# Kernel tuning notes

Hardware: AMD Instinct MI355X
Metric: run time of the kernel (lower is better)

Reference implementation:

```python
import jax, jax.numpy as jnp
import numpy as np


def _lstm_cell(x, h, c, Wih, Whh, b):
    # torch LSTM gate order: i, f, g, o
    g = x @ Wih.T + h @ Whh.T + b
    i, f, gg, o = jnp.split(g, 4, axis=-1)
    c = jax.nn.sigmoid(f) * c + jax.nn.sigmoid(i) * jnp.tanh(gg)
    h = jax.nn.sigmoid(o) * jnp.tanh(c)
    return h, c


def _run_lstm(emb, mask, Wih, Whh, b, reverse):
    # mask-gated scan emulates pack_padded_sequence: state frozen on pad steps,
    # final (h, c) equals state at last valid token of each sequence.
    B = emb.shape[0]
    H = Whh.shape[1]
    def step(carry, inp):
        h, c = carry
        x, m = inp  # x: (B, E), m: (B, 1)
        hn, cn = _lstm_cell(x, h, c, Wih, Whh, b)
        h = m * hn + (1.0 - m) * h
        c = m * cn + (1.0 - m) * c
        return (h, c), h
    xs = (jnp.swapaxes(emb, 0, 1), jnp.swapaxes(mask, 0, 1)[..., None])
    z = jnp.zeros((B, H), emb.dtype)
    (h, c), outs = jax.lax.scan(step, (z, z), xs, reverse=reverse)
    return jnp.swapaxes(outs, 0, 1), h, c  # (B, T, H), (B, H), (B, H)


def setup_inputs() -> dict:
    key = jax.random.key(0)
    ks = iter(jax.random.split(key, 40))
    B, Te, Td, E, H, Ve, Vd = 32, 64, 32, 256, 512, 32000, 32000
    s = 0.05
    def rn(shape):
        return jax.random.normal(next(ks), shape, jnp.float32) * s
    def zz(n):
        return jnp.zeros((n,), jnp.float32)
    return {
        "enc_texts": jax.random.randint(next(ks), (B, Te), 0, Ve),
        "enc_mask": jnp.ones((B, Te), jnp.float32),
        "dec_texts": jax.random.randint(next(ks), (B, Td), 0, Vd),
        "enc_emb": rn((Ve, E)),
        "dec_emb": rn((Vd, E)),
        "Wih_f": rn((4 * H, E)), "Whh_f": rn((4 * H, H)), "b_f": zz(4 * H),
        "Wih_b": rn((4 * H, E)), "Whh_b": rn((4 * H, H)), "b_b": zz(4 * H),
        "Wih_d": rn((4 * H, E + 2 * H)), "Whh_d": rn((4 * H, H)), "b_d": zz(4 * H),
        "W_h": rn((H, 2 * H)), "b_h": zz(H),
        "W_c": rn((H, 2 * H)), "b_c": zz(H),
        "W_df": rn((2 * H, 2 * H)), "b_df": zz(2 * H),
        "W_ef": rn((2 * H, 2 * H)), "b_ef": zz(2 * H),
        "W_out": rn((Vd, 3 * H)), "b_out": zz(Vd),
    }


def reference(enc_texts, enc_mask, dec_texts, enc_emb, dec_emb,
              Wih_f, Whh_f, b_f, Wih_b, Whh_b, b_b,
              Wih_d, Whh_d, b_d, W_h, b_h, W_c, b_c,
              W_df, b_df, W_ef, b_ef, W_out, b_out):
    B = enc_texts.shape[0]
    H = Whh_d.shape[1]
    # ---- encode: bidirectional LSTM over embedded source ----
    emb = enc_emb[enc_texts]  # (B, Te, E)
    out_f, hf, cf = _run_lstm(emb, enc_mask, Wih_f, Whh_f, b_f, reverse=False)
    out_b, hb, cb = _run_lstm(emb, enc_mask, Wih_b, Whh_b, b_b, reverse=True)
    enc_output = jnp.concatenate([out_f, out_b], -1) * enc_mask[..., None]  # (B, Te, 2H)
    # ---- decode_init: project concat of directional final states ----
    dec_h = jax.nn.relu(jnp.concatenate([hf, hb], -1) @ W_h.T + b_h)  # (B, H)
    dec_c = jax.nn.relu(jnp.concatenate([cf, cb], -1) @ W_c.T + b_c)  # (B, H)
    # precompute attention keys once (enc_output_fc)
    enc_feat = enc_output @ W_ef.T + b_ef  # (B, Te, 2H)
    # teacher-forcing inputs: tokens 0..Td-2
    dec_in = dec_emb[dec_texts[:, :-1]]  # (B, Td-1, E)
    ctx0 = jnp.zeros((B, 2 * H), enc_output.dtype)

    def step(carry, x):
        h, c, ctx = carry
        xin = jnp.concatenate([x, ctx], -1)  # (B, E + 2H)
        h, c = _lstm_cell(xin, h, c, Wih_d, Whh_d, b_d)
        # dot attention: query from projected (h, c)
        df = jnp.concatenate([h, c], -1) @ W_df.T + b_df  # (B, 2H)
        scores = jnp.einsum('bd,btd->bt', df, enc_feat)
        a = jax.nn.softmax(scores, axis=-1) * enc_mask
        a = a / jnp.sum(a, axis=-1, keepdims=True)
        ctx = jnp.einsum('bt,btd->bd', a, enc_output)  # (B, 2H)
        logits = jnp.concatenate([h, ctx], -1) @ W_out.T + b_out  # (B, Vd)
        return (h, c, ctx), logits

    _, logits = jax.lax.scan(step, (dec_h, dec_c, ctx0), jnp.swapaxes(dec_in, 0, 1))
    return jnp.swapaxes(logits, 0, 1)  # (B, Td-1, Vd)
```

## Files before the change

### kernel.cpp

```cpp
#include <hip/hip_runtime.h>
#include <hip/hip_bf16.h>


typedef __attribute__((ext_vector_type(8))) short bfrag_t;
typedef __attribute__((ext_vector_type(4))) float f4_t;

static __device__ __forceinline__ float bf2f(unsigned short u) {
  union { float f; unsigned int i; } v; v.i = ((unsigned int)u) << 16; return v.f;
}
static __device__ __forceinline__ unsigned short f2bf(float f) {
  union { float f; unsigned int i; } v; v.f = f;
  unsigned int r = v.i + 0x7FFFu + ((v.i >> 16) & 1u);
  return (unsigned short)(r >> 16);
}
static __device__ __forceinline__ unsigned int pack_bf2(float lo, float hi) {
  __hip_bfloat162 h2 = __float22bfloat162_rn(make_float2(lo, hi));
  union { __hip_bfloat162 h; unsigned int u; } cv; cv.h = h2;
  return cv.u;
}
static __device__ __forceinline__ float sigm(float x) {
  return __builtin_amdgcn_rcpf(1.f + __expf(-x));
}
static __device__ __forceinline__ float ftanh(float x) {
  float e = __expf(2.f * x);
  return 1.f - 2.f * __builtin_amdgcn_rcpf(e + 1.f);
}

#define GLDS16(g, l)                                                        \
  __builtin_amdgcn_global_load_lds(                                         \
      (const __attribute__((address_space(1))) void*)(g),                   \
      (__attribute__((address_space(3))) void*)(l), 16, 0, 0)

static __device__ __forceinline__ void st_f32_coh(float* p, float v) {
  asm volatile("global_store_dword %0, %1, off sc0 sc1" :: "v"(p), "v"(v) : "memory");
}
static __device__ __forceinline__ void st_u16_coh(unsigned short* p, unsigned short x) {
  asm volatile("global_store_short %0, %1, off sc0 sc1" :: "v"(p), "v"((unsigned)x) : "memory");
}
static __device__ __forceinline__ float ld_f32_coh(const float* p) {
  float v;
  asm volatile("global_load_dword %0, %1, off sc0 sc1\n\ts_waitcnt vmcnt(0)"
               : "=v"(v) : "v"(p) : "memory");
  return v;
}

static __device__ __forceinline__ void arrive8(unsigned* base) {
  __syncthreads();
  if (threadIdx.x == 0)
    __hip_atomic_fetch_add(base + (blockIdx.x & 7) * 32, 1u,
                           __ATOMIC_RELAXED, __HIP_MEMORY_SCOPE_AGENT);
}
static __device__ __forceinline__ void wait8(unsigned* base, unsigned target) {
  if (threadIdx.x < 64) {
    unsigned sum;
    do {
      unsigned v = 0;
      if (threadIdx.x < 8)
        v = __hip_atomic_load(base + threadIdx.x * 32,
                              __ATOMIC_RELAXED, __HIP_MEMORY_SCOPE_AGENT);
      v += __shfl_xor(v, 1);
      v += __shfl_xor(v, 2);
      v += __shfl_xor(v, 4);
      sum = __shfl(v, 0);
      if (sum < target) __builtin_amdgcn_s_sleep(2);
    } while (sum < target);
  }
  __syncthreads();
}
static __device__ __forceinline__ void gbar8(unsigned* base, unsigned target) {
  arrive8(base);
  wait8(base, target);
}

__global__ __launch_bounds__(256) void gemm_bt_kernel(
    const unsigned short* __restrict__ A, int lda,
    const float* __restrict__ B, int ldb, int bcol0,
    const float* __restrict__ bias, void* __restrict__ Cv, int ldc,
    int Mvalid, int K, int Mt, int swz, int obf) {
  __shared__ unsigned short As[128 * 32];
  __shared__ unsigned short Bs[128 * 32];
  int id = blockIdx.x;
  if (swz) { int x = id & 7; id = x * ((int)gridDim.x >> 3) + (id >> 3); }
  const int mb = id % Mt, nb = id / Mt;
  const int m0 = mb * 128, n0 = nb * 128;
  const int tid = threadIdx.x;
  const int w = tid >> 6, lane = tid & 63;
  const int wr = (w >> 1) * 64, wc = (w & 1) * 64;
  const int l15 = lane & 15, l4 = lane >> 4;

  const int arow = w * 16 + (lane >> 2);
  const int acol = (lane & 3) * 8;
  const unsigned short* Ag = A + (size_t)(m0 + arow) * lda + acol;

  const int brow = tid >> 1;
  const int bcol = (tid & 1) * 16;
  const float* Bg = B + (size_t)(n0 + brow) * ldb + bcol0 + bcol;
  unsigned short* Bsw = Bs + brow * 32 + bcol;

  f4_t acc[4][4];
#pragma unroll
  for (int i = 0; i < 4; ++i)
#pragma unroll
    for (int j = 0; j < 4; ++j) {
      acc[i][j].x = 0.f; acc[i][j].y = 0.f; acc[i][j].z = 0.f; acc[i][j].w = 0.f;
    }

  for (int kt = 0; kt < K; kt += 32) {
    GLDS16(Ag + kt, As + w * 512);
    GLDS16(Ag + (size_t)64 * lda + kt, As + (4 + w) * 512);
    float4 q0 = *(const float4*)(Bg + kt);
    float4 q1 = *(const float4*)(Bg + kt + 4);
    float4 q2 = *(const float4*)(Bg + kt + 8);
    float4 q3 = *(const float4*)(Bg + kt + 12);
    union { unsigned int u[8]; uint4 q[2]; } pk;
    pk.u[0] = pack_bf2(q0.x, q0.y); pk.u[1] = pack_bf2(q0.z, q0.w);
    pk.u[2] = pack_bf2(q1.x, q1.y); pk.u[3] = pack_bf2(q1.z, q1.w);
    pk.u[4] = pack_bf2(q2.x, q2.y); pk.u[5] = pack_bf2(q2.z, q2.w);
    pk.u[6] = pack_bf2(q3.x, q3.y); pk.u[7] = pack_bf2(q3.z, q3.w);
    *(uint4*)(Bsw) = pk.q[0];
    *(uint4*)(Bsw + 8) = pk.q[1];
    __syncthreads();
    bfrag_t af[4], bfv[4];
#pragma unroll
    for (int m = 0; m < 4; ++m)
      af[m] = *(const bfrag_t*)(As + (wr + m * 16 + l15) * 32 + l4 * 8);
#pragma unroll
    for (int n = 0; n < 4; ++n)
      bfv[n] = *(const bfrag_t*)(Bs + (wc + n * 16 + l15) * 32 + l4 * 8);
#pragma unroll
    for (int m = 0; m < 4; ++m)
#pragma unroll
      for (int n = 0; n < 4; ++n)
        acc[m][n] = __builtin_amdgcn_mfma_f32_16x16x32_bf16(af[m], bfv[n], acc[m][n], 0, 0, 0);
    __syncthreads();
  }

  const int crb = l4 * 4;
  float* Cf = (float*)Cv;
  unsigned short* Ch = (unsigned short*)Cv;
#pragma unroll
  for (int m = 0; m < 4; ++m)
#pragma unroll
    for (int n = 0; n < 4; ++n)
#pragma unroll
      for (int r = 0; r < 4; ++r) {
        int gr = m0 + wr + m * 16 + crb + r;
        if (gr < Mvalid) {
          int gc = n0 + wc + n * 16 + l15;
          float v = acc[m][n][r] + (bias ? bias[gc] : 0.f);
          if (obf) Ch[(size_t)gr * ldc + gc] = f2bf(v);
          else     Cf[(size_t)gr * ldc + gc] = v;
        }
      }
}

__global__ void gather_enc_kernel(const int* __restrict__ texts,
                                  const float* __restrict__ table,
                                  unsigned short* __restrict__ out) {
  const int row = blockIdx.x;
  const int tok = texts[row];
  const float4 v = *(const float4*)(table + (size_t)tok * 256 + threadIdx.x * 4);
  unsigned short* o = out + (size_t)row * 256 + threadIdx.x * 4;
  o[0] = f2bf(v.x); o[1] = f2bf(v.y); o[2] = f2bf(v.z); o[3] = f2bf(v.w);
}

__global__ void gather_dec_kernel(const int* __restrict__ texts,
                                  const float* __restrict__ table,
                                  unsigned short* __restrict__ out) {
  const int row = blockIdx.x;
  unsigned short* o = out + (size_t)row * 256 + threadIdx.x * 4;
  if (row >= 992) { o[0] = 0; o[1] = 0; o[2] = 0; o[3] = 0; return; }
  const int b = row / 31, t2 = row - b * 31;
  const int tok = texts[b * 32 + t2];
  const float4 v = *(const float4*)(table + (size_t)tok * 256 + threadIdx.x * 4);
  o[0] = f2bf(v.x); o[1] = f2bf(v.y); o[2] = f2bf(v.z); o[3] = f2bf(v.w);
}

__global__ __launch_bounds__(256) void wdf_t_kernel(
    const float* __restrict__ W_df, const float* __restrict__ b_df,
    float* __restrict__ WT) {
  const int bid = blockIdx.x;
  if (bid < 1024) {
    __shared__ float tl[32][33];
    const int tx = (bid & 31) * 32, ty = (bid >> 5) * 32;
    const int r = threadIdx.x >> 5, c = threadIdx.x & 31;
#pragma unroll
    for (int i = 0; i < 4; ++i)
      tl[r + i * 8][c] = W_df[(size_t)(ty + r + i * 8) * 1024 + tx + c];
    __syncthreads();
#pragma unroll
    for (int i = 0; i < 4; ++i)
      WT[(size_t)(tx + r + i * 8) * 1024 + ty + c] = tl[c][r + i * 8];
  } else {
    for (int i = threadIdx.x; i < 1024; i += 256)
      WT[(size_t)1024 * 1024 + i] = b_df[i];
  }
}

__global__ __launch_bounds__(256) void mega_enc_kernel(
    const float* __restrict__ XF, const float* __restrict__ XB,
    const float* __restrict__ Whh_f, const float* __restrict__ Whh_b,
    const float* __restrict__ mask,
    unsigned short* __restrict__ HBF,
    unsigned short* __restrict__ ENCO, float* __restrict__ HFIN,
    unsigned* bar) {
  const int bi = blockIdx.x;
  const int dir = bi >> 6;
  const int u0 = (bi & 63) * 8;
  const int tid = threadIdx.x;
  const float* X = dir ? XB : XF;
  const float* W = dir ? Whh_b : Whh_f;
  unsigned short* Hbf = HBF + dir * 32768;
  unsigned* cnt = bar + dir * 256;

  __shared__ unsigned short WA[32 * 520];
  __shared__ unsigned short HB[32 * 520];
  __shared__ float Gl[32][33];

#pragma unroll
  for (int i = 0; i < 16; ++i) {
    int idx = tid + i * 256;
    int r = idx >> 7, c4 = idx & 127;
    const float4 v = *(const float4*)(W + (size_t)((r >> 3) * 512 + u0 + (r & 7)) * 512 + c4 * 4);
    *(uint2*)(WA + r * 520 + c4 * 4) = make_uint2(pack_bf2(v.x, v.y), pack_bf2(v.z, v.w));
  }
  __syncthreads();

  const int w = tid >> 6, lane = tid & 63;
  const int l15 = lane & 15, l4 = lane >> 4;
  const int wrow = (w >> 1) * 16, wcol = (w & 1) * 16;

  bfrag_t afr[16];
#pragma unroll
  for (int kk = 0; kk < 16; ++kk)
    afr[kk] = *(const bfrag_t*)(WA + (wrow + l15) * 520 + kk * 32 + l4 * 8);

  const int ob = tid & 31, ouo = tid >> 5;
  const int ou = u0 + ouo;
  float h_reg = 0.f, c_reg = 0.f;

  unsigned tgt = 0;
  for (int s = 0; s < 64; ++s) {
    const int t = dir ? (63 - s) : s;
    const int pp = s & 1;
    const float* xp = X + ((size_t)ob * 64 + t) * 2048 + ou;
    float xg0 = xp[0], xg1 = xp[512], xg2 = xp[1024], xg3 = xp[1536];
    float mval = mask[ob * 64 + t];
    const unsigned short* hsrc = Hbf + pp * 16384;
    uint4 tmp[8];
#pragma unroll
    for (int i = 0; i < 8; ++i) {
      int idx = tid + i * 256;
      int r = idx >> 6, c = idx & 63;
      asm volatile("global_load_dwordx4 %0, %1, off sc0 sc1"
                   : "=v"(tmp[i]) : "v"(hsrc + r * 512 + c * 8));
    }
    asm volatile("s_waitcnt vmcnt(0)" ::: "memory");
#pragma unroll
    for (int i = 0; i < 8; ++i) {
      int idx = tid + i * 256;
      int r = idx >> 6, c = idx & 63;
      *(uint4*)(HB + r * 520 + c * 8) = tmp[i];
    }
    __syncthreads();
    {
      f4_t ae = {0.f, 0.f, 0.f, 0.f}, ao = {0.f, 0.f, 0.f, 0.f};
#pragma unroll
      for (int kk = 0; kk < 16; kk += 2) {
        bfrag_t b0 = *(const bfrag_t*)(HB + (wcol + l15) * 520 + kk * 32 + l4 * 8);
        bfrag_t b1 = *(const bfrag_t*)(HB + (wcol + l15) * 520 + (kk + 1) * 32 + l4 * 8);
        ae = __builtin_amdgcn_mfma_f32_16x16x32_bf16(afr[kk], b0, ae, 0, 0, 0);
        ao = __builtin_amdgcn_mfma_f32_16x16x32_bf16(afr[kk + 1], b1, ao, 0, 0, 0);
      }
#pragma unroll
      for (int r = 0; r < 4; ++r)
        Gl[wrow + l4 * 4 + r][wcol + l15] = ae[r] + ao[r];
    }
    __syncthreads();
    {
      float gi = Gl[ouo][ob] + xg0;
      float gf = Gl[8 + ouo][ob] + xg1;
      float gg = Gl[16 + ouo][ob] + xg2;
      float go = Gl[24 + ouo][ob] + xg3;
      float cn = sigm(gf) * c_reg + sigm(gi) * ftanh(gg);
      float hn = sigm(go) * ftanh(cn);
      float hmix = mval * hn + (1.f - mval) * h_reg;
      float cmix = mval * cn + (1.f - mval) * c_reg;
      h_reg = hmix; c_reg = cmix;
      ENCO[((size_t)ob * 64 + t) * 1024 + dir * 512 + ou] = f2bf(hmix * mval);
      st_u16_coh(Hbf + (pp ^ 1) * 16384 + ob * 512 + ou, f2bf(hmix));
      if (s == 63) {
        HFIN[dir * 16384 + ob * 512 + ou] = hmix;
        HFIN[(2 + dir) * 16384 + ob * 512 + ou] = cmix;
      }
    }
    if (s < 63) { tgt += 64; gbar8(cnt, tgt); }
  }
}

__global__ __launch_bounds__(256) void mega_dec_kernel(
    const float* __restrict__ HFIN, const float* __restrict__ W_h,
    const float* __restrict__ b_h, const float* __restrict__ W_c,
    const float* __restrict__ b_c, const float* __restrict__ XD,
    const float* __restrict__ Wih_d, const float* __restrict__ Whh_d,
    const unsigned short* __restrict__ EFG, const unsigned short* __restrict__ ENCO,
    const float* __restrict__ mask, float* __restrict__ DECH,
    float* __restrict__ DECC, unsigned short* __restrict__ PRE0,
    unsigned short* __restrict__ ACAT, unsigned* bar) {
  const int bi = blockIdx.x;
  const int tid = threadIdx.x;
  const bool is_attn = (bi >= 128);
  const int u0 = bi * 4;
  unsigned* barB1 = bar;
  unsigned* barB2 = bar + 256;

  __shared__ union {
    struct {
      unsigned short wga[16 * 1544];
      unsigned short xb[32 * 1544];
      float gl[16][33];
    } s;
    struct {
      unsigned short efg[64 * 1160];
      float hcl[1024];
      float scl[64];
      float al[64];
    } a;
    struct { float xl[32][132]; float wi[8][132]; } ini;
  } U;

  const int ob = tid & 31, ouo = (tid >> 5) & 3, ou = u0 + ouo;
  const int w = tid >> 6, lane = tid & 63;
  const int l15 = lane & 15, l4 = lane >> 4;

  if (!is_attn) {
    {
      const int mat = bi >> 6, j0i = (bi & 63) * 8;
      const int jj = tid >> 5, b = tid & 31;
      const int sr = tid >> 5, sc = (tid & 31) * 4;
      const float* Wm = mat ? W_c : W_h;
      const float* bias = mat ? b_c : b_h;
      const float* x0 = HFIN + (size_t)(mat ? 2 : 0) * 16384;
      const float* x1 = HFIN + (size_t)(mat ? 3 : 1) * 16384;
      float acc = 0.f;
      for (int kc = 0; kc < 1024; kc += 128) {
#pragma unroll
        for (int i = 0; i < 4; ++i) {
          int r = sr + i * 8;
          const float* src = (kc < 512) ? (x0 + r * 512 + kc + sc)
                                        : (x1 + r * 512 + (kc - 512) + sc);
          *(float4*)&U.ini.xl[r][sc] = *(const float4*)src;
        }
        *(float4*)&U.ini.wi[sr][sc] = *(const float4*)(Wm + (size_t)(j0i + sr) * 1024 + kc + sc);
        __syncthreads();
#pragma unroll
        for (int k = 0; k < 128; k += 4) {
          float4 wv = *(const float4*)&U.ini.wi[jj][k];
          float4 xv = *(const float4*)&U.ini.xl[b][k];
          acc += wv.x * xv.x + wv.y * xv.y + wv.z * xv.z + wv.w * xv.w;
        }
        __syncthreads();
      }
      float v = fmaxf(acc + bias[j0i + jj], 0.f);
      if (mat == 0) {
        st_f32_coh(DECH + b * 512 + j0i + jj, v);
        st_u16_coh(PRE0 + (size_t)b * 1536 + j0i + jj, f2bf(v));
      } else {
        st_f32_coh(DECC + b * 512 + j0i + jj, v);
      }
    }
    arrive8(barB1);
    wait8(barB1, 128);

#pragma unroll
    for (int i = 0; i < 24; ++i) {
      int idx = tid + i * 256;
      int r = idx / 384, c4 = idx - (idx / 384) * 384;
      int wrow = (r >> 2) * 512 + u0 + (r & 3);
      int c = c4 * 4;
      float4 v;
      if (c < 512) v = *(const float4*)(Whh_d + (size_t)wrow * 512 + c);
      else         v = *(const float4*)(Wih_d + (size_t)wrow * 1280 + 256 + (c - 512));
      *(uint2*)(U.s.wga + r * 1544 + c) = make_uint2(pack_bf2(v.x, v.y), pack_bf2(v.z, v.w));
    }
    float h_reg = 0.f, c_reg = 0.f;
    if (tid < 128) {
      h_reg = ld_f32_coh(DECH + ob * 512 + ou);
      c_reg = ld_f32_coh(DECC + ob * 512 + ou);
    }

    f4_t cae = {0.f, 0.f, 0.f, 0.f}, cao = {0.f, 0.f, 0.f, 0.f};

    for (int t = 0; t < 31; ++t) {
      float xg0 = 0, xg1 = 0, xg2 = 0, xg3 = 0;
      if (tid < 128) {
        const float* xp = XD + ((size_t)ob * 31 + t) * 2048 + ou;
        xg0 = xp[0]; xg1 = xp[512]; xg2 = xp[1024]; xg3 = xp[1536];
      }
      if (t == 0) {
        uint4 tmp[24];
#pragma unroll
        for (int i = 0; i < 24; ++i) {
          int idx = tid + i * 256;
          int r = idx / 192, c16 = idx - (idx / 192) * 192;
          asm volatile("global_load_dwordx4 %0, %1, off sc0 sc1"
                       : "=v"(tmp[i]) : "v"(PRE0 + (size_t)r * 1536 + c16 * 8));
        }
        asm volatile("s_waitcnt vmcnt(0)" ::: "memory");
#pragma unroll
        for (int i = 0; i < 24; ++i) {
          int idx = tid + i * 256;
          int r = idx / 192, c16 = idx - (idx / 192) * 192;
          *(uint4*)(U.s.xb + r * 1544 + c16 * 8) = tmp[i];
        }
        __syncthreads();
        if (w < 2) {
          f4_t ae = {0.f, 0.f, 0.f, 0.f}, ao = {0.f, 0.f, 0.f, 0.f};
#pragma unroll
          for (int kk = 0; kk < 48; kk += 2) {
            bfrag_t a0 = *(const bfrag_t*)(U.s.wga + l15 * 1544 + kk * 32 + l4 * 8);
            bfrag_t b0 = *(const bfrag_t*)(U.s.xb + (w * 16 + l15) * 1544 + kk * 32 + l4 * 8);
            bfrag_t a1 = *(const bfrag_t*)(U.s.wga + l15 * 1544 + (kk + 1) * 32 + l4 * 8);
            bfrag_t b1 = *(const bfrag_t*)(U.s.xb + (w * 16 + l15) * 1544 + (kk + 1) * 32 + l4 * 8);
            ae = __builtin_amdgcn_mfma_f32_16x16x32_bf16(a0, b0, ae, 0, 0, 0);
            ao = __builtin_amdgcn_mfma_f32_16x16x32_bf16(a1, b1, ao, 0, 0, 0);
          }
#pragma unroll
          for (int r = 0; r < 4; ++r)
            U.s.gl[l4 * 4 + r][w * 16 + l15] = ae[r] + ao[r];
        }
      } else {
        wait8(barB2, 32u * t);
        uint4 tmp[16];
#pragma unroll
        for (int i = 0; i < 16; ++i) {
          int idx = tid + i * 256;
          int r = idx >> 7, c16 = 64 + (idx & 127);
          asm volatile("global_load_dwordx4 %0, %1, off sc0 sc1"
                       : "=v"(tmp[i]) : "v"(ACAT + ((size_t)r * 31 + (t - 1)) * 1536 + c16 * 8));
        }
        asm volatile("s_waitcnt vmcnt(8)" ::: "memory");
#pragma unroll
        for (int i = 0; i < 8; ++i) {
          int idx = tid + i * 256;
          int r = idx >> 7, c16 = 64 + (idx & 127);
          *(uint4*)(U.s.xb + r * 1544 + c16 * 8) = tmp[i];
        }
        asm volatile("s_waitcnt vmcnt(0)" ::: "memory");
#pragma unroll
        for (int i = 8; i < 16; ++i) {
          int idx = tid + i * 256;
          int r = idx >> 7, c16 = 64 + (idx & 127);
          *(uint4*)(U.s.xb + r * 1544 + c16 * 8) = tmp[i];
        }
        __syncthreads();
        if (w < 2) {
          f4_t ae = cae, ao = cao;
#pragma unroll
          for (int kk = 16; kk < 48; kk += 2) {
            bfrag_t a0 = *(const bfrag_t*)(U.s.wga + l15 * 1544 + kk * 32 + l4 * 8);
            bfrag_t b0 = *(const bfrag_t*)(U.s.xb + (w * 16 + l15) * 1544 + kk * 32 + l4 * 8);
            bfrag_t a1 = *(const bfrag_t*)(U.s.wga + l15 * 1544 + (kk + 1) * 32 + l4 * 8);
            bfrag_t b1 = *(const bfrag_t*)(U.s.xb + (w * 16 + l15) * 1544 + (kk + 1) * 32 + l4 * 8);
            ae = __builtin_amdgcn_mfma_f32_16x16x32_bf16(a0, b0, ae, 0, 0, 0);
            ao = __builtin_amdgcn_mfma_f32_16x16x32_bf16(a1, b1, ao, 0, 0, 0);
          }
#pragma unroll
          for (int r = 0; r < 4; ++r)
            U.s.gl[l4 * 4 + r][w * 16 + l15] = ae[r] + ao[r];
        }
      }
      __syncthreads();
      if (tid < 128) {
        float gi = U.s.gl[ouo][ob] + xg0;
        float gf = U.s.gl[4 + ouo][ob] + xg1;
        float gg = U.s.gl[8 + ouo][ob] + xg2;
        float go = U.s.gl[12 + ouo][ob] + xg3;
        float cn = sigm(gf) * c_reg + sigm(gi) * ftanh(gg);
        float hn = sigm(go) * ftanh(cn);
        h_reg = hn; c_reg = cn;
        st_f32_coh(DECH + ob * 512 + ou, hn);
        st_f32_coh(DECC + ob * 512 + ou, cn);
        st_u16_coh(ACAT + ((size_t)ob * 31 + t) * 1536 + ou, f2bf(hn));
      }
      arrive8(barB1);
      if (t < 30) {
        wait8(barB1, 128u * (t + 2));
        uint4 pre[8];
#pragma unroll
        for (int i = 0; i < 8; ++i) {
          int idx = tid + i * 256;
          int r = idx >> 6, c16 = idx & 63;
          asm volatile("global_load_dwordx4 %0, %1, off sc0 sc1"
                       : "=v"(pre[i]) : "v"(ACAT + ((size_t)r * 31 + t) * 1536 + c16 * 8));
        }
        asm volatile("s_waitcnt vmcnt(0)" ::: "memory");
#pragma unroll
        for (int i = 0; i < 8; ++i) {
          int idx = tid + i * 256;
          int r = idx >> 6, c16 = idx & 63;
          *(uint4*)(U.s.xb + r * 1544 + c16 * 8) = pre[i];
        }
        __syncthreads();
        if (w < 2) {
          f4_t ae = {0.f, 0.f, 0.f, 0.f}, ao = {0.f, 0.f, 0.f, 0.f};
#pragma unroll
          for (int kk = 0; kk < 16; kk += 2) {
            bfrag_t a0 = *(const bfrag_t*)(U.s.wga + l15 * 1544 + kk * 32 + l4 * 8);
            bfrag_t b0 = *(const bfrag_t*)(U.s.xb + (w * 16 + l15) * 1544 + kk * 32 + l4 * 8);
            bfrag_t a1 = *(const bfrag_t*)(U.s.wga + l15 * 1544 + (kk + 1) * 32 + l4 * 8);
            bfrag_t b1 = *(const bfrag_t*)(U.s.xb + (w * 16 + l15) * 1544 + (kk + 1) * 32 + l4 * 8);
            ae = __builtin_amdgcn_mfma_f32_16x16x32_bf16(a0, b0, ae, 0, 0, 0);
            ao = __builtin_amdgcn_mfma_f32_16x16x32_bf16(a1, b1, ao, 0, 0, 0);
          }
          cae = ae; cao = ao;
        }
      }
    }
  } else {
    const int b = bi - 128;
    for (int idx = tid; idx < 64 * 144; idx += 256) {
      int s = idx / 144, c16 = idx - (idx / 144) * 144;
      *(uint4*)(U.a.efg + s * 1160 + c16 * 8) =
          *(const uint4*)(EFG + ((size_t)b * 64 + s) * 1152 + c16 * 8);
    }
    for (int t = 0; t < 31; ++t) {
      wait8(barB1, 128u * (t + 2));
      {
        int c = tid * 4;
        const float* hp = (c < 512) ? (DECH + b * 512 + c) : (DECC + b * 512 + (c - 512));
        uint4 hv;
        asm volatile("global_load_dwordx4 %0, %1, off sc0 sc1\n\ts_waitcnt vmcnt(0)"
                     : "=v"(hv) : "v"(hp) : "memory");
        *(uint4*)&U.a.hcl[c] = hv;
      }
      __syncthreads();
      {
        const int sidx = tid >> 2, part = tid & 3;
        const unsigned short* eg = U.a.efg + sidx * 1160 + part * 256;
        const float* d = &U.a.hcl[part * 256];
        float acc = 0.f;
#pragma unroll 8
        for (int k = 0; k < 256; k += 8) {
          uint4 v = *(const uint4*)(eg + k);
          acc += bf2f((unsigned short)(v.x & 0xFFFFu)) * d[k + 0];
          acc += bf2f((unsigned short)(v.x >> 16))     * d[k + 1];
          acc += bf2f((unsigned short)(v.y & 0xFFFFu)) * d[k + 2];
          acc += bf2f((unsigned short)(v.y >> 16))     * d[k + 3];
          acc += bf2f((unsigned short)(v.z & 0xFFFFu)) * d[k + 4];
          acc += bf2f((unsigned short)(v.z >> 16))     * d[k + 5];
          acc += bf2f((unsigned short)(v.w & 0xFFFFu)) * d[k + 6];
          acc += bf2f((unsigned short)(v.w >> 16))     * d[k + 7];
        }
        acc += __shfl_xor(acc, 1);
        acc += __shfl_xor(acc, 2);
        if (part == 0)
          U.a.scl[sidx] = acc + bf2f(U.a.efg[sidx * 1160 + 1024]);
      }
      __syncthreads();
      if (tid < 64) {
        float v = U.a.scl[tid];
        float mx = v;
#pragma unroll
        for (int o = 32; o >= 1; o >>= 1) mx = fmaxf(mx, __shfl_xor(mx, o));
        float e = __expf(v - mx) * mask[b * 64 + tid];
        float sm = e;
#pragma unroll
        for (int o = 32; o >= 1; o >>= 1) sm += __shfl_xor(sm, o);
        U.a.al[tid] = e / sm;
      }
      __syncthreads();
      float c0 = 0.f, c1 = 0.f, c2 = 0.f, c3 = 0.f;
#pragma unroll 8
      for (int tp = 0; tp < 64; ++tp) {
        float a = U.a.al[tp];
        const unsigned short* eo = ENCO + ((size_t)b * 64 + tp) * 1024 + tid;
        c0 += a * bf2f(eo[0]);
        c1 += a * bf2f(eo[256]);
        c2 += a * bf2f(eo[512]);
        c3 += a * bf2f(eo[768]);
      }
      unsigned short* ap = ACAT + ((size_t)b * 31 + t) * 1536 + 512;
      st_u16_coh(ap + tid, f2bf(c0));
      st_u16_coh(ap + tid + 256, f2bf(c1));
      st_u16_coh(ap + tid + 512, f2bf(c2));
      st_u16_coh(ap + tid + 768, f2bf(c3));
      arrive8(barB2);
    }
  }
}

extern "C" void kernel_launch(void* const* d_in, const int* in_sizes, int n_in,
                              void* d_out, int out_size, void* d_ws, size_t ws_size,
                              hipStream_t stream) {
  const int*   enc_texts = (const int*)  d_in[0];
  const float* enc_mask  = (const float*)d_in[1];
  const int*   dec_texts = (const int*)  d_in[2];
  const float* enc_emb   = (const float*)d_in[3];
  const float* dec_emb   = (const float*)d_in[4];
  const float* Wih_f = (const float*)d_in[5];
  const float* Whh_f = (const float*)d_in[6];
  const float* b_f   = (const float*)d_in[7];
  const float* Wih_b = (const float*)d_in[8];
  const float* Whh_b = (const float*)d_in[9];
  const float* b_b   = (const float*)d_in[10];
  const float* Wih_d = (const float*)d_in[11];
  const float* Whh_d = (const float*)d_in[12];
  const float* b_d   = (const float*)d_in[13];
  const float* W_h   = (const float*)d_in[14];
  const float* b_h   = (const float*)d_in[15];
  const float* W_c   = (const float*)d_in[16];
  const float* b_c   = (const float*)d_in[17];
  const float* W_df  = (const float*)d_in[18];
  const float* b_df  = (const float*)d_in[19];
  const float* W_ef  = (const float*)d_in[20];
  const float* b_ef  = (const float*)d_in[21];
  const float* W_out = (const float*)d_in[22];
  const float* b_out = (const float*)d_in[23];
  float* out = (float*)d_out;

  char* ws = (char*)d_ws;
  size_t off = 0;
  auto alloc = [&](size_t bytes) {
    char* p = ws + off;
    off += (bytes + 255) & ~(size_t)255;
    return p;
  };
  unsigned short* HBF  = (unsigned short*)alloc((size_t)2 * 2 * 16384 * 2);
  float* DECH = (float*)alloc((size_t)16384 * 4);
  float* DECC = (float*)alloc((size_t)16384 * 4);
  unsigned short* PRE0 = (unsigned short*)alloc((size_t)32 * 1536 * 2);
  unsigned short* ACAT = (unsigned short*)alloc((size_t)1024 * 1536 * 2);
  unsigned* bar = (unsigned*)alloc(4096);
  unsigned* barD = bar + 512;
  size_t zbytes = off;
  float* XF = (float*)alloc((size_t)2048 * 2048 * 4);
  float* XB = (float*)alloc((size_t)2048 * 2048 * 4);
  float* XD = (float*)alloc((size_t)1024 * 2048 * 4);
  unsigned short* EFb  = (unsigned short*)alloc((size_t)2048 * 1024 * 2);
  unsigned short* ENCO = (unsigned short*)alloc((size_t)2048 * 1024 * 2);
  unsigned short* EMBB = (unsigned short*)alloc((size_t)2048 * 256 * 2);
  unsigned short* DEMB = (unsigned short*)alloc((size_t)1024 * 256 * 2);
  float* HFIN = (float*)alloc((size_t)4 * 16384 * 4);
  unsigned short* EFG = (unsigned short*)XF;
  float* WT  = XB;

  hipMemsetAsync(d_ws, 0, zbytes, stream);

  gather_enc_kernel<<<2048, 64, 0, stream>>>(enc_texts, enc_emb, EMBB);
  gather_dec_kernel<<<1024, 64, 0, stream>>>(dec_texts, dec_emb, DEMB);

  dim3 blk(256);
  gemm_bt_kernel<<<256, blk, 0, stream>>>(EMBB, 256, Wih_f, 256, 0, b_f, XF, 2048, 2048, 256, 16, 0, 0);
  gemm_bt_kernel<<<256, blk, 0, stream>>>(EMBB, 256, Wih_b, 256, 0, b_b, XB, 2048, 2048, 256, 16, 0, 0);
  gemm_bt_kernel<<<128, blk, 0, stream>>>(DEMB, 256, Wih_d, 1280, 0, b_d, XD, 2048, 1024, 256, 8, 0, 0);

  mega_enc_kernel<<<128, blk, 0, stream>>>(XF, XB, Whh_f, Whh_b, enc_mask, HBF, ENCO, HFIN, bar);

  wdf_t_kernel<<<1025, blk, 0, stream>>>(W_df, b_df, WT);
  gemm_bt_kernel<<<128, blk, 0, stream>>>(ENCO, 1024, W_ef, 1024, 0, b_ef, EFb, 1024, 2048, 1024, 16, 0, 1);
  gemm_bt_kernel<<<144, blk, 0, stream>>>(EFb, 1024, WT, 1024, 0, nullptr, EFG, 1152, 2048, 1024, 16, 0, 1);

  mega_dec_kernel<<<160, blk, 0, stream>>>(HFIN, W_h, b_h, W_c, b_c, XD, Wih_d, Whh_d,
                                           EFG, ENCO, enc_mask, DECH, DECC, PRE0, ACAT, barD);

  gemm_bt_kernel<<<2000, blk, 0, stream>>>(ACAT, 1536, W_out, 1536, 0, b_out, out, 32000, 992, 1536, 8, 1, 0);
}
```

Before: 1.248 ms.

## Load decoder B operands directly into registers and split K across four waves

The decoder recurrence blocks no longer stage the activation matrix in shared memory. Each wave loads its own B fragments straight from global memory into registers. All four waves now run MFMAs, each covering one K-half for one batch group, and the partial gate sums are added during the cell update. The early partial product over the h part after the B1 barrier is removed, so the whole K=1536 reduction now happens after waiting on the attention barrier. This trades the earlier overlap for more MFMA parallelism, less LDS traffic and fewer syncthreads per step.

```diff
diff --git a/kernel.cpp b/kernel.cpp
--- a/kernel.cpp
+++ b/kernel.cpp
@@ -317,8 +317,7 @@
   __shared__ union {
     struct {
       unsigned short wga[16 * 1544];
-      unsigned short xb[32 * 1544];
-      float gl[16][33];
+      float gl[2][16][33];
     } s;
     struct {
       unsigned short efg[64 * 1160];
@@ -388,8 +387,12 @@
       h_reg = ld_f32_coh(DECH + ob * 512 + ou);
       c_reg = ld_f32_coh(DECC + ob * 512 + ou);
     }
-
-    f4_t cae = {0.f, 0.f, 0.f, 0.f}, cao = {0.f, 0.f, 0.f, 0.f};
+    __syncthreads();
+
+    const int khalf = w >> 1;
+    const int bg = w & 1;
+    const int brow_f = bg * 16 + l15;
+    const int kbase = khalf * 768 + l4 * 8;
 
     for (int t = 0; t < 31; ++t) {
       float xg0 = 0, xg1 = 0, xg2 = 0, xg3 = 0;
@@ -397,85 +400,36 @@
         const float* xp = XD + ((size_t)ob * 31 + t) * 2048 + ou;
         xg0 = xp[0]; xg1 = xp[512]; xg2 = xp[1024]; xg3 = xp[1536];
       }
-      if (t == 0) {
-        uint4 tmp[24];
-#pragma unroll
-        for (int i = 0; i < 24; ++i) {
-          int idx = tid + i * 256;
-          int r = idx / 192, c16 = idx - (idx / 192) * 192;
-          asm volatile("global_load_dwordx4 %0, %1, off sc0 sc1"
-                       : "=v"(tmp[i]) : "v"(PRE0 + (size_t)r * 1536 + c16 * 8));
+      if (t > 0) wait8(barB2, 32u * t);
+      const unsigned short* bp = (t == 0)
+          ? (PRE0 + (size_t)brow_f * 1536 + kbase)
+          : (ACAT + ((size_t)brow_f * 31 + (t - 1)) * 1536 + kbase);
+      union { uint4 u; bfrag_t b; } bf[24];
+#pragma unroll
+      for (int j = 0; j < 24; ++j)
+        asm volatile("global_load_dwordx4 %0, %1, off sc0 sc1"
+                     : "=v"(bf[j].u) : "v"(bp + j * 32));
+      asm volatile("s_waitcnt vmcnt(0)" ::: "memory");
+      {
+        f4_t ae = {0.f, 0.f, 0.f, 0.f}, ao = {0.f, 0.f, 0.f, 0.f};
+#pragma unroll
+        for (int j = 0; j < 24; j += 2) {
+          int kk = khalf * 24 + j;
+          bfrag_t a0 = *(const bfrag_t*)(U.s.wga + l15 * 1544 + kk * 32 + l4 * 8);
+          bfrag_t a1 = *(const bfrag_t*)(U.s.wga + l15 * 1544 + (kk + 1) * 32 + l4 * 8);
+          ae = __builtin_amdgcn_mfma_f32_16x16x32_bf16(a0, bf[j].b, ae, 0, 0, 0);
+          ao = __builtin_amdgcn_mfma_f32_16x16x32_bf16(a1, bf[j + 1].b, ao, 0, 0, 0);
         }
-        asm volatile("s_waitcnt vmcnt(0)" ::: "memory");
-#pragma unroll
-        for (int i = 0; i < 24; ++i) {
-          int idx = tid + i * 256;
-          int r = idx / 192, c16 = idx - (idx / 192) * 192;
-          *(uint4*)(U.s.xb + r * 1544 + c16 * 8) = tmp[i];
-        }
-        __syncthreads();
-        if (w < 2) {
-          f4_t ae = {0.f, 0.f, 0.f, 0.f}, ao = {0.f, 0.f, 0.f, 0.f};
-#pragma unroll
-          for (int kk = 0; kk < 48; kk += 2) {
-            bfrag_t a0 = *(const bfrag_t*)(U.s.wga + l15 * 1544 + kk * 32 + l4 * 8);
-            bfrag_t b0 = *(const bfrag_t*)(U.s.xb + (w * 16 + l15) * 1544 + kk * 32 + l4 * 8);
-            bfrag_t a1 = *(const bfrag_t*)(U.s.wga + l15 * 1544 + (kk + 1) * 32 + l4 * 8);
-            bfrag_t b1 = *(const bfrag_t*)(U.s.xb + (w * 16 + l15) * 1544 + (kk + 1) * 32 + l4 * 8);
-            ae = __builtin_amdgcn_mfma_f32_16x16x32_bf16(a0, b0, ae, 0, 0, 0);
-            ao = __builtin_amdgcn_mfma_f32_16x16x32_bf16(a1, b1, ao, 0, 0, 0);
-          }
-#pragma unroll
-          for (int r = 0; r < 4; ++r)
-            U.s.gl[l4 * 4 + r][w * 16 + l15] = ae[r] + ao[r];
-        }
-      } else {
-        wait8(barB2, 32u * t);
-        uint4 tmp[16];
-#pragma unroll
-        for (int i = 0; i < 16; ++i) {
-          int idx = tid + i * 256;
-          int r = idx >> 7, c16 = 64 + (idx & 127);
-          asm volatile("global_load_dwordx4 %0, %1, off sc0 sc1"
-                       : "=v"(tmp[i]) : "v"(ACAT + ((size_t)r * 31 + (t - 1)) * 1536 + c16 * 8));
-        }
-        asm volatile("s_waitcnt vmcnt(8)" ::: "memory");
-#pragma unroll
-        for (int i = 0; i < 8; ++i) {
-          int idx = tid + i * 256;
-          int r = idx >> 7, c16 = 64 + (idx & 127);
-          *(uint4*)(U.s.xb + r * 1544 + c16 * 8) = tmp[i];
-        }
-        asm volatile("s_waitcnt vmcnt(0)" ::: "memory");
-#pragma unroll
-        for (int i = 8; i < 16; ++i) {
-          int idx = tid + i * 256;
-          int r = idx >> 7, c16 = 64 + (idx & 127);
-          *(uint4*)(U.s.xb + r * 1544 + c16 * 8) = tmp[i];
-        }
-        __syncthreads();
-        if (w < 2) {
-          f4_t ae = cae, ao = cao;
-#pragma unroll
-          for (int kk = 16; kk < 48; kk += 2) {
-            bfrag_t a0 = *(const bfrag_t*)(U.s.wga + l15 * 1544 + kk * 32 + l4 * 8);
-            bfrag_t b0 = *(const bfrag_t*)(U.s.xb + (w * 16 + l15) * 1544 + kk * 32 + l4 * 8);
-            bfrag_t a1 = *(const bfrag_t*)(U.s.wga + l15 * 1544 + (kk + 1) * 32 + l4 * 8);
-            bfrag_t b1 = *(const bfrag_t*)(U.s.xb + (w * 16 + l15) * 1544 + (kk + 1) * 32 + l4 * 8);
-            ae = __builtin_amdgcn_mfma_f32_16x16x32_bf16(a0, b0, ae, 0, 0, 0);
-            ao = __builtin_amdgcn_mfma_f32_16x16x32_bf16(a1, b1, ao, 0, 0, 0);
-          }
-#pragma unroll
-          for (int r = 0; r < 4; ++r)
-            U.s.gl[l4 * 4 + r][w * 16 + l15] = ae[r] + ao[r];
-        }
+#pragma unroll
+        for (int r = 0; r < 4; ++r)
+          U.s.gl[khalf][l4 * 4 + r][bg * 16 + l15] = ae[r] + ao[r];
       }
       __syncthreads();
       if (tid < 128) {
-        float gi = U.s.gl[ouo][ob] + xg0;
-        float gf = U.s.gl[4 + ouo][ob] + xg1;
-        float gg = U.s.gl[8 + ouo][ob] + xg2;
-        float go = U.s.gl[12 + ouo][ob] + xg3;
+        float gi = U.s.gl[0][ouo][ob]      + U.s.gl[1][ouo][ob]      + xg0;
+        float gf = U.s.gl[0][4 + ouo][ob]  + U.s.gl[1][4 + ouo][ob]  + xg1;
+        float gg = U.s.gl[0][8 + ouo][ob]  + U.s.gl[1][8 + ouo][ob]  + xg2;
+        float go = U.s.gl[0][12 + ouo][ob] + U.s.gl[1][12 + ouo][ob] + xg3;
         float cn = sigm(gf) * c_reg + sigm(gi) * ftanh(gg);
         float hn = sigm(go) * ftanh(cn);
         h_reg = hn; c_reg = cn;
@@ -484,38 +438,6 @@
         st_u16_coh(ACAT + ((size_t)ob * 31 + t) * 1536 + ou, f2bf(hn));
       }
       arrive8(barB1);
-      if (t < 30) {
-        wait8(barB1, 128u * (t + 2));
-        uint4 pre[8];
-#pragma unroll
-        for (int i = 0; i < 8; ++i) {
-          int idx = tid + i * 256;
-          int r = idx >> 6, c16 = idx & 63;
-          asm volatile("global_load_dwordx4 %0, %1, off sc0 sc1"
-                       : "=v"(pre[i]) : "v"(ACAT + ((size_t)r * 31 + t) * 1536 + c16 * 8));
-        }
-        asm volatile("s_waitcnt vmcnt(0)" ::: "memory");
-#pragma unroll
-        for (int i = 0; i < 8; ++i) {
-          int idx = tid + i * 256;
-          int r = idx >> 6, c16 = idx & 63;
-          *(uint4*)(U.s.xb + r * 1544 + c16 * 8) = pre[i];
-        }
-        __syncthreads();
-        if (w < 2) {
-          f4_t ae = {0.f, 0.f, 0.f, 0.f}, ao = {0.f, 0.f, 0.f, 0.f};
-#pragma unroll
-          for (int kk = 0; kk < 16; kk += 2) {
-            bfrag_t a0 = *(const bfrag_t*)(U.s.wga + l15 * 1544 + kk * 32 + l4 * 8);
-            bfrag_t b0 = *(const bfrag_t*)(U.s.xb + (w * 16 + l15) * 1544 + kk * 32 + l4 * 8);
-            bfrag_t a1 = *(const bfrag_t*)(U.s.wga + l15 * 1544 + (kk + 1) * 32 + l4 * 8);
-            bfrag_t b1 = *(const bfrag_t*)(U.s.xb + (w * 16 + l15) * 1544 + (kk + 1) * 32 + l4 * 8);
-            ae = __builtin_amdgcn_mfma_f32_16x16x32_bf16(a0, b0, ae, 0, 0, 0);
-            ao = __builtin_amdgcn_mfma_f32_16x16x32_bf16(a1, b1, ao, 0, 0, 0);
-          }
-          cae = ae; cao = ao;
-        }
-      }
     }
   } else {
     const int b = bi - 128;
```

Measured after the change: 1.277 ms. 1.02x slower.
